# Optimization experiments

Hardware: AMD Instinct MI355X
Metric: run time of the kernel (lower is better)

The kernel has to match this reference:

```python
import jax, jax.numpy as jnp
import numpy as np

EMBED_DIM = 1024
NUM_HEADS = 16
HEAD_DIM = EMBED_DIM // NUM_HEADS
TGT_LEN = 1024
SRC_LEN = 1024
BSZ = 4


def setup_inputs() -> dict:
    key = jax.random.key(0)
    ks = jax.random.split(key, 7)
    query = jax.random.normal(ks[0], (TGT_LEN, BSZ, EMBED_DIM), dtype=jnp.float32)
    key_t = jax.random.normal(ks[1], (SRC_LEN, BSZ, EMBED_DIM), dtype=jnp.float32)
    # hard 0/1 multiplicative mask applied post-softmax
    hard_attention = jax.random.randint(ks[2], (BSZ, TGT_LEN, SRC_LEN), 0, 2).astype(jnp.float32)
    # xavier_uniform_ on [3E, E]
    limit = float(np.sqrt(6.0 / (3 * EMBED_DIM + EMBED_DIM)))
    in_proj_weight = jax.random.uniform(ks[3], (3 * EMBED_DIM, EMBED_DIM), dtype=jnp.float32,
                                        minval=-limit, maxval=limit)
    in_proj_bias = jnp.zeros((3 * EMBED_DIM,), dtype=jnp.float32)
    limit_o = float(np.sqrt(1.0 / EMBED_DIM))
    out_proj_weight = jax.random.uniform(ks[4], (EMBED_DIM, EMBED_DIM), dtype=jnp.float32,
                                         minval=-limit_o, maxval=limit_o)
    out_proj_bias = jnp.zeros((EMBED_DIM,), dtype=jnp.float32)
    return {
        "query": query,
        "key": key_t,
        "hard_attention": hard_attention,
        "in_proj_weight": in_proj_weight,
        "in_proj_bias": in_proj_bias,
        "out_proj_weight": out_proj_weight,
        "out_proj_bias": out_proj_bias,
    }


def reference(query, key, hard_attention, in_proj_weight, in_proj_bias,
              out_proj_weight, out_proj_bias):
    tgt_len, bsz, embed_dim = query.shape
    src_len = key.shape[0]
    h, hd = NUM_HEADS, embed_dim // NUM_HEADS
    scaling = float(hd) ** -0.5

    # QKV projections (F.linear uses y = x @ W.T + b)
    wq = in_proj_weight[:embed_dim]
    wkv = in_proj_weight[embed_dim:]
    bq = in_proj_bias[:embed_dim]
    bkv = in_proj_bias[embed_dim:]
    q = jnp.einsum('tbe,fe->tbf', query, wq) + bq          # [T,B,E]
    kv = jnp.einsum('sbe,fe->sbf', key, wkv) + bkv          # [S,B,2E]
    k, v = jnp.split(kv, 2, axis=-1)

    q = (q * scaling).reshape(tgt_len, bsz, h, hd).transpose(1, 2, 0, 3)  # [B,H,T,D]
    k = k.reshape(src_len, bsz, h, hd).transpose(1, 2, 0, 3)              # [B,H,S,D]
    v = v.reshape(src_len, bsz, h, hd).transpose(1, 2, 0, 3)              # [B,H,S,D]

    scores = jnp.einsum('bhtd,bhsd->bhts', q, k)            # [B,H,T,S]
    attn = jax.nn.softmax(scores, axis=-1)
    # dropout_p = 0.0 -> identity
    attn = attn * hard_attention[:, None, :, :]             # post-softmax hard mask

    out = jnp.einsum('bhts,bhsd->bhtd', attn, v)            # [B,H,T,D]
    out = out.transpose(2, 0, 1, 3).reshape(tgt_len, bsz, embed_dim)
    out = jnp.einsum('tbe,fe->tbf', out, out_proj_weight) + out_proj_bias

    avg_weights = attn.sum(axis=1) / h                      # [B,T,S]
    return (out, avg_weights)
```

## Files before the change

### kernel.cpp

```cpp
#include <hip/hip_runtime.h>
#include <cstdint>
#include <cstddef>

typedef __bf16 bf16x8 __attribute__((ext_vector_type(8)));
typedef float  f32x4  __attribute__((ext_vector_type(4)));
typedef unsigned short u16x8 __attribute__((ext_vector_type(8)));

__device__ __forceinline__ uint16_t f2bf(float f) {
  uint32_t u = __float_as_uint(f);
  u += 0x7fffu + ((u >> 16) & 1u);
  return (uint16_t)(u >> 16);
}
__device__ __forceinline__ float bf2f(uint16_t u) {
  return __uint_as_float((uint32_t)u << 16);
}
__device__ __forceinline__ uint32_t cvtpk(float lo, float hi) {
  uint32_t r;
  asm("v_cvt_pk_bf16_f32 %0, %1, %2" : "=v"(r) : "v"(lo), "v"(hi));
  return r;
}

__device__ __forceinline__ f32x4 mfma16(bf16x8 a, bf16x8 b, f32x4 c) {
  return __builtin_amdgcn_mfma_f32_16x16x32_bf16(a, b, c, 0, 0, 0);
}

#define GLD_TO_LDS16(gptr, lptr)                                                   \
  __builtin_amdgcn_global_load_lds(                                                \
      (const __attribute__((address_space(1))) void*)(gptr),                       \
      (__attribute__((address_space(3))) void*)(lptr), 16, 0, 0)

__global__ void cvt_all(const float* __restrict__ q, const float* __restrict__ k,
                        const float* __restrict__ w, const float* __restrict__ wo,
                        uint16_t* __restrict__ Xq, uint16_t* __restrict__ Xk,
                        uint16_t* __restrict__ Wb, uint16_t* __restrict__ Wob) {
  int i = blockIdx.x * blockDim.x + threadIdx.x;
  const float* src;
  uint16_t* dst;
  int off;
  if (i < 1048576)      { src = q;  dst = Xq;  off = i; }
  else if (i < 2097152) { src = k;  dst = Xk;  off = i - 1048576; }
  else if (i < 2883584) { src = w;  dst = Wb;  off = i - 2097152; }
  else                  { src = wo; dst = Wob; off = i - 2883584; }
  float4 v = ((const float4*)src)[off];
  ushort4 o;
  o.x = f2bf(v.x); o.y = f2bf(v.y); o.z = f2bf(v.z); o.w = f2bf(v.w);
  ((ushort4*)dst)[off] = o;
}

__global__ void bitpack(const float* __restrict__ hard, uint32_t* __restrict__ bits) {
  int i = blockIdx.x * 256 + threadIdx.x;
  unsigned long long m = __ballot(hard[i] != 0.0f);
  if ((threadIdx.x & 63) == 0) {
    int w = i >> 5;
    bits[w]     = (uint32_t)m;
    bits[w + 1] = (uint32_t)(m >> 32);
  }
}

__global__ __launch_bounds__(256)
void gemm_qkv(const uint16_t* __restrict__ Xq, const uint16_t* __restrict__ Xk,
              const uint16_t* __restrict__ Wb, const float* __restrict__ ipb,
              uint16_t* __restrict__ Qb, uint16_t* __restrict__ Kb,
              uint16_t* __restrict__ Vt) {
  __shared__ __align__(16) uint16_t As[128 * 32];
  __shared__ __align__(16) uint16_t Bs[128 * 32];
  const int tid  = threadIdx.x;
  const int wave = tid >> 6, lane = tid & 63;
  const int quad = lane >> 4, l16 = lane & 15;

  const int bid = blockIdx.x;
  const uint16_t *A, *B;
  const float* bias;
  int bm, bn, mode;
  if (bid < 256) {
    mode = 0; A = Xq; B = Wb; bias = ipb;
    bm = bid >> 3; bn = bid & 7;
  } else {
    mode = 1; A = Xk; B = Wb + (1 << 20); bias = ipb + 1024;
    int t = bid - 256; bm = t >> 4; bn = t & 15;
  }
  const int wm = (wave >> 1) << 6, wn = (wave & 1) << 6;
  const int K = 1024;

  f32x4 acc[4][4] = {};

  for (int k0 = 0; k0 < K; k0 += 32) {
    __syncthreads();
#pragma unroll
    for (int j = 0; j < 2; j++) {
      int c   = wave * 128 + j * 64 + lane;
      int row = c >> 2, kc = c & 3;
      const uint16_t* ga = A + (size_t)(bm * 128 + row) * K + k0 + kc * 8;
      GLD_TO_LDS16(ga, As + (size_t)(wave * 128 + j * 64) * 8);
      const uint16_t* gb = B + (size_t)(bn * 128 + row) * K + k0 + kc * 8;
      GLD_TO_LDS16(gb, Bs + (size_t)(wave * 128 + j * 64) * 8);
    }
    __syncthreads();

    bf16x8 af[4], bfr[4];
#pragma unroll
    for (int i = 0; i < 4; i++) {
      af[i]  = *(const bf16x8*)(As + (wm + i * 16 + l16) * 32 + quad * 8);
      bfr[i] = *(const bf16x8*)(Bs + (wn + i * 16 + l16) * 32 + quad * 8);
    }
#pragma unroll
    for (int mi = 0; mi < 4; mi++)
#pragma unroll
      for (int ni = 0; ni < 4; ni++)
        acc[mi][ni] = mfma16(af[mi], bfr[ni], acc[mi][ni]);
  }

#pragma unroll
  for (int mi = 0; mi < 4; mi++)
#pragma unroll
    for (int ni = 0; ni < 4; ni++)
#pragma unroll
      for (int r = 0; r < 4; r++) {
        int gi = bm * 128 + wm + mi * 16 + quad * 4 + r;
        int gf = bn * 128 + wn + ni * 16 + l16;
        float c = acc[mi][ni][r] + bias[gf];
        if (mode == 0) {
          c *= 0.125f;
          int t = gi >> 2, b = gi & 3, h = gf >> 6, d = gf & 63;
          Qb[((((size_t)b * 16 + h) * 1024 + t) << 6) + d] = f2bf(c);
        } else {
          int s = gi >> 2, b = gi & 3;
          if (gf < 1024) {
            int h = gf >> 6, d = gf & 63;
            Kb[((((size_t)b * 16 + h) * 1024 + s) << 6) + d] = f2bf(c);
          } else {
            int fv = gf - 1024, h = fv >> 6, d = fv & 63;
            Vt[((((size_t)b * 16 + h) * 64 + d) << 10) + s] = f2bf(c);
          }
        }
      }
}

__global__ __launch_bounds__(256)
void gemm_out(const uint16_t* __restrict__ A, const uint16_t* __restrict__ B,
              const float* __restrict__ bias, float* __restrict__ o32) {
  __shared__ __align__(16) uint16_t As[64 * 32];
  __shared__ __align__(16) uint16_t Bs[128 * 32];
  const int tid  = threadIdx.x;
  const int wave = tid >> 6, lane = tid & 63;
  const int quad = lane >> 4, l16 = lane & 15;
  const int bm = blockIdx.x >> 3, bn = blockIdx.x & 7;
  const int wm = (wave >> 1) << 5, wn = (wave & 1) << 6;
  const int K = 1024;

  f32x4 acc[2][4] = {};

  for (int k0 = 0; k0 < K; k0 += 32) {
    __syncthreads();
    {
      int c   = wave * 64 + lane;
      int row = c >> 2, kc = c & 3;
      const uint16_t* ga = A + (size_t)(bm * 64 + row) * K + k0 + kc * 8;
      GLD_TO_LDS16(ga, As + (size_t)(wave * 64) * 8);
    }
#pragma unroll
    for (int j = 0; j < 2; j++) {
      int c   = wave * 128 + j * 64 + lane;
      int row = c >> 2, kc = c & 3;
      const uint16_t* gb = B + (size_t)(bn * 128 + row) * K + k0 + kc * 8;
      GLD_TO_LDS16(gb, Bs + (size_t)(wave * 128 + j * 64) * 8);
    }
    __syncthreads();

    bf16x8 af[2], bfr[4];
#pragma unroll
    for (int i = 0; i < 2; i++)
      af[i] = *(const bf16x8*)(As + (wm + i * 16 + l16) * 32 + quad * 8);
#pragma unroll
    for (int i = 0; i < 4; i++)
      bfr[i] = *(const bf16x8*)(Bs + (wn + i * 16 + l16) * 32 + quad * 8);
#pragma unroll
    for (int mi = 0; mi < 2; mi++)
#pragma unroll
      for (int ni = 0; ni < 4; ni++)
        acc[mi][ni] = mfma16(af[mi], bfr[ni], acc[mi][ni]);
  }

#pragma unroll
  for (int mi = 0; mi < 2; mi++)
#pragma unroll
    for (int ni = 0; ni < 4; ni++)
#pragma unroll
      for (int r = 0; r < 4; r++) {
        int gi = bm * 64 + wm + mi * 16 + quad * 4 + r;
        int gf = bn * 128 + wn + ni * 16 + l16;
        o32[(size_t)gi * 1024 + gf] = acc[mi][ni][r] + bias[gf];
      }
}

__global__ __launch_bounds__(256, 2)
void attn_kernel(const uint16_t* __restrict__ qb, const uint16_t* __restrict__ kb,
                 const uint16_t* __restrict__ vtb, const uint32_t* __restrict__ bits,
                 uint16_t* __restrict__ attn_out, float* __restrict__ rlout) {
  __shared__ __align__(16) uint16_t Ks[128 * 64];
  __shared__ __align__(16) uint16_t Vs[64 * 128];
  __shared__ __align__(16) uint16_t Pb[4 * 32 * 128];

  const int bid = blockIdx.x;
  const int xcd = bid & 7, j = bid >> 3;
  const int slab = xcd * 8 + (j >> 3);
  const int b = slab >> 4, h = slab & 15;
  const int t0 = (j & 7) << 7;
  const int tid = threadIdx.x, wave = tid >> 6, lane = tid & 63;
  const int quad = lane >> 4, l16 = lane & 15;
  const int sw = (l16 & 7) << 4;
  const size_t bh = (size_t)b * 16 + h;
  const int tw = t0 + wave * 32;
  const int ta = tw + l16, tb = ta + 16;
  char* PwA = (char*)(Pb + wave * (32 * 128)) + l16 * 256;
  char* PwB = PwA + 16 * 256;

  const uint16_t* qA = qb + ((bh << 10) + ta) * 64;
  bf16x8 aqA0 = *(const bf16x8*)(qA + quad * 8);
  bf16x8 aqA1 = *(const bf16x8*)(qA + 32 + quad * 8);
  bf16x8 aqB0 = *(const bf16x8*)(qA + 1024 + quad * 8);
  bf16x8 aqB1 = *(const bf16x8*)(qA + 1024 + 32 + quad * 8);

  f32x4 accA[4] = {}, accB[4] = {};
  float smA = 0.f, smB = 0.f;

  const int kr = tid >> 3, kc8 = tid & 7;
  const int vr = tid >> 4, vc16 = tid & 15;

  const uint32_t* bA = bits + (((size_t)(b << 10) + ta) << 5);
  const uint32_t* bB = bits + (((size_t)(b << 10) + tb) << 5);

  u16x8 kreg[4], vreg[4];
#pragma unroll
  for (int r = 0; r < 4; r++)
    kreg[r] = *(const u16x8*)(kb + (bh << 16) + (size_t)(r * 256 + tid) * 8);
#pragma unroll
  for (int r = 0; r < 4; r++)
    vreg[r] = *(const u16x8*)(vtb + (((bh << 6) + r * 16 + vr) << 10) + vc16 * 8);
  uint4 uA = *(const uint4*)bA;
  uint4 uB = *(const uint4*)bB;

  for (int sc = 0; sc < 8; sc++) {
    uint32_t wA[4] = {uA.x >> (quad * 4), uA.y >> (quad * 4),
                      uA.z >> (quad * 4), uA.w >> (quad * 4)};
    uint32_t wB[4] = {uB.x >> (quad * 4), uB.y >> (quad * 4),
                      uB.z >> (quad * 4), uB.w >> (quad * 4)};

    __syncthreads();
#pragma unroll
    for (int r = 0; r < 4; r++) {
      const int row = r * 32 + kr;
      *(u16x8*)((char*)Ks + row * 128 + ((kc8 * 16) ^ ((row & 7) << 4))) = kreg[r];
    }
#pragma unroll
    for (int r = 0; r < 4; r++) {
      const int row = r * 16 + vr;
      *(u16x8*)((char*)Vs + row * 256 + ((vc16 * 16) ^ ((row & 7) << 4))) = vreg[r];
    }
    __syncthreads();

    if (sc < 7) {
      const uint16_t* kbase = kb + (bh << 16) + (size_t)(sc + 1) * 8192;
#pragma unroll
      for (int r = 0; r < 4; r++)
        kreg[r] = *(const u16x8*)(kbase + (size_t)(r * 256 + tid) * 8);
#pragma unroll
      for (int r = 0; r < 4; r++)
        vreg[r] = *(const u16x8*)(vtb + (((bh << 6) + r * 16 + vr) << 10) +
                                  (sc + 1) * 128 + vc16 * 8);
      uA = *(const uint4*)(bA + (sc + 1) * 4);
      uB = *(const uint4*)(bB + (sc + 1) * 4);
    }

#pragma unroll
    for (int nn = 0; nn < 8; nn++) {
      const char* kbp = (const char*)Ks + (nn * 16 + l16) * 128;
      bf16x8 bk0 = *(const bf16x8*)(kbp + ((quad * 16) ^ sw));
      bf16x8 bk1 = *(const bf16x8*)(kbp + ((64 + quad * 16) ^ sw));
      f32x4 cA = {}, cB = {};
      cA = mfma16(bk0, aqA0, cA); cA = mfma16(bk1, aqA1, cA);
      cB = mfma16(bk0, aqB0, cB); cB = mfma16(bk1, aqB1, cB);
      const uint32_t mA = wA[nn >> 1] >> ((nn & 1) * 16);
      const uint32_t mB = wB[nn >> 1] >> ((nn & 1) * 16);
      float eA[4], eB[4];
#pragma unroll
      for (int r = 0; r < 4; r++) {
        eA[r] = __expf(cA[r]); smA += eA[r];
        eB[r] = __expf(cB[r]); smB += eB[r];
        eA[r] = ((mA >> r) & 1) ? eA[r] : 0.f;
        eB[r] = ((mB >> r) & 1) ? eB[r] : 0.f;
      }
      const int pc = (nn * 32 + quad * 8) ^ sw;
      *(uint2*)(PwA + pc) = make_uint2(cvtpk(eA[0], eA[1]), cvtpk(eA[2], eA[3]));
      *(uint2*)(PwB + pc) = make_uint2(cvtpk(eB[0], eB[1]), cvtpk(eB[2], eB[3]));
    }

#pragma unroll
    for (int kc = 0; kc < 4; kc++) {
      const int pcb = (kc * 64 + quad * 16) ^ sw;
      bf16x8 apA = *(const bf16x8*)(PwA + pcb);
      bf16x8 apB = *(const bf16x8*)(PwB + pcb);
#pragma unroll
      for (int dt = 0; dt < 4; dt++) {
        bf16x8 bv = *(const bf16x8*)((const char*)Vs + (dt * 16 + l16) * 256 +
                                     ((kc * 64 + quad * 16) ^ sw));
        accA[dt] = mfma16(bv, apA, accA[dt]);
        accB[dt] = mfma16(bv, apB, accB[dt]);
      }
    }
  }

  smA += __shfl_xor(smA, 16); smA += __shfl_xor(smA, 32);
  smB += __shfl_xor(smB, 16); smB += __shfl_xor(smB, 32);
  const float rlA = 1.0f / smA, rlB = 1.0f / smB;
  if (quad == 0) rlout[(bh << 10) + ta] = rlA;
  if (quad == 1) rlout[(bh << 10) + tb] = rlB;

#pragma unroll
  for (int dt = 0; dt < 4; dt++) {
    uint2 oA = make_uint2(cvtpk(accA[dt][0] * rlA, accA[dt][1] * rlA),
                          cvtpk(accA[dt][2] * rlA, accA[dt][3] * rlA));
    *(uint2*)(attn_out + ((size_t)(ta * 4 + b) << 10) + h * 64 + dt * 16 + quad * 4) = oA;
    uint2 oB = make_uint2(cvtpk(accB[dt][0] * rlB, accB[dt][1] * rlB),
                          cvtpk(accB[dt][2] * rlB, accB[dt][3] * rlB));
    *(uint2*)(attn_out + ((size_t)(tb * 4 + b) << 10) + h * 64 + dt * 16 + quad * 4) = oB;
  }
}

__global__ __launch_bounds__(256, 2)
void avg_kernel(const uint16_t* __restrict__ qb, const uint16_t* __restrict__ kb,
                const float* __restrict__ rlin, const uint32_t* __restrict__ bits,
                float* __restrict__ avgout) {
  __shared__ __align__(16) uint16_t Ks[128 * 64];

  const int bid = blockIdx.x;
  const int xcd = bid & 7, j = bid >> 3;
  const int b  = xcd >> 1;
  const int t0 = ((xcd & 1) * 8 + (j >> 3)) << 6;
  const int s0 = (j & 7) << 7;
  const int tid = threadIdx.x, wave = tid >> 6, lane = tid & 63;
  const int quad = lane >> 4, l16 = lane & 15;
  const int sw = (l16 & 7) << 4;
  const int tr = t0 + wave * 16 + l16;
  const int kr = tid >> 3, kc8 = tid & 7;

  uint4 u = *(const uint4*)(bits + (((size_t)(b << 10) + tr) << 5) + (s0 >> 5));
  uint32_t w4[4] = {u.x >> (quad * 4), u.y >> (quad * 4),
                    u.z >> (quad * 4), u.w >> (quad * 4)};

  float av[8][4] = {};

  u16x8 kreg[4];
  {
    const uint16_t* kb0 = kb + ((((size_t)b * 16) << 10) + s0) * 64;
#pragma unroll
    for (int r = 0; r < 4; r++)
      kreg[r] = *(const u16x8*)(kb0 + (size_t)(r * 256 + tid) * 8);
  }

  for (int hh = 0; hh < 16; hh++) {
    __syncthreads();
#pragma unroll
    for (int r = 0; r < 4; r++) {
      const int row = r * 32 + kr;
      *(u16x8*)((char*)Ks + row * 128 + ((kc8 * 16) ^ ((row & 7) << 4))) = kreg[r];
    }
    __syncthreads();
    if (hh < 15) {
      const uint16_t* kb2 = kb + ((((size_t)b * 16 + hh + 1) << 10) + s0) * 64;
#pragma unroll
      for (int r = 0; r < 4; r++)
        kreg[r] = *(const u16x8*)(kb2 + (size_t)(r * 256 + tid) * 8);
    }

    const size_t bh = (size_t)b * 16 + hh;
    const uint16_t* qrow = qb + ((bh << 10) + tr) * 64;
    bf16x8 aq0 = *(const bf16x8*)(qrow + quad * 8);
    bf16x8 aq1 = *(const bf16x8*)(qrow + 32 + quad * 8);
    const float rl = rlin[(bh << 10) + tr];

#pragma unroll
    for (int n = 0; n < 8; n++) {
      const char* kbp = (const char*)Ks + (n * 16 + l16) * 128;
      bf16x8 bk0 = *(const bf16x8*)(kbp + ((quad * 16) ^ sw));
      bf16x8 bk1 = *(const bf16x8*)(kbp + ((64 + quad * 16) ^ sw));
      f32x4 c = {};
      c = mfma16(bk0, aq0, c);
      c = mfma16(bk1, aq1, c);
#pragma unroll
      for (int r = 0; r < 4; r++) av[n][r] += __expf(c[r]) * rl;
    }
  }

  float* orow = avgout + ((size_t)(b << 10) + tr) * 1024 + s0 + quad * 4;
#pragma unroll
  for (int n = 0; n < 8; n++) {
    const uint32_t m = w4[n >> 1] >> ((n & 1) * 16);
    float4 f;
    f.x = av[n][0] * (((m >> 0) & 1) ? 0.0625f : 0.f);
    f.y = av[n][1] * (((m >> 1) & 1) ? 0.0625f : 0.f);
    f.z = av[n][2] * (((m >> 2) & 1) ? 0.0625f : 0.f);
    f.w = av[n][3] * (((m >> 3) & 1) ? 0.0625f : 0.f);
    *(float4*)(orow + n * 16) = f;
  }
}

extern "C" void kernel_launch(void* const* d_in, const int* in_sizes, int n_in,
                              void* d_out, int out_size, void* d_ws, size_t ws_size,
                              hipStream_t stream) {
  const float* query = (const float*)d_in[0];
  const float* key   = (const float*)d_in[1];
  const float* hard  = (const float*)d_in[2];
  const float* ipw   = (const float*)d_in[3];
  const float* ipb   = (const float*)d_in[4];
  const float* opw   = (const float*)d_in[5];
  const float* opb   = (const float*)d_in[6];

  char* ws = (char*)d_ws;
  const size_t MB = 1ull << 20;
  uint16_t* Xq  = (uint16_t*)(ws + 0);
  uint16_t* Xk  = (uint16_t*)(ws + 8 * MB);
  uint16_t* Wb  = (uint16_t*)(ws + 16 * MB);
  uint16_t* Wob = (uint16_t*)(ws + 22 * MB);
  uint16_t* Qb  = (uint16_t*)(ws + 24 * MB);
  uint16_t* Kb  = (uint16_t*)(ws + 32 * MB);
  uint16_t* Vt  = (uint16_t*)(ws + 40 * MB);
  uint16_t* AO  = Xq;

  float* out = (float*)d_out;
  float* avg = out + 4194304;
  uint32_t* bits  = (uint32_t*)out;
  float*    rlbuf = out + 131072;

  cvt_all<<<12288, 256, 0, stream>>>(query, key, ipw, opw, Xq, Xk, Wb, Wob);
  bitpack<<<16384, 256, 0, stream>>>(hard, bits);

  gemm_qkv<<<768, 256, 0, stream>>>(Xq, Xk, Wb, ipb, Qb, Kb, Vt);

  attn_kernel<<<512, 256, 0, stream>>>(Qb, Kb, Vt, bits, AO, rlbuf);

  avg_kernel<<<512, 256, 0, stream>>>(Qb, Kb, rlbuf, bits, avg);

  gemm_out<<<512, 256, 0, stream>>>(AO, Wob, opb, out);
}
```

Baseline: 242.0 us.

## Rewrite QKV GEMM with 256x256 tiles, double-buffered swizzled LDS, and 8 waves

Replaces the 128x128 single-buffered QKV projection GEMM with a 256x256 tile kernel running 8 waves per block. The K dimension is staged in 64-wide tiles through double-buffered LDS with an XOR swizzle, and global-to-LDS prefetch of the next tile is interleaved with MFMA phases. The kernel also raises wave priority during the MFMA phases and remaps block ids for L2 locality. The aim is better operand reuse, fewer global loads, fewer bank conflicts, and load latency hidden behind compute. The cost is that only 192 blocks are launched, which may underfill the GPU, and the 128KB LDS footprint limits occupancy.

```diff
diff --git a/kernel.cpp b/kernel.cpp
--- a/kernel.cpp
+++ b/kernel.cpp
@@ -57,80 +57,131 @@
   }
 }
 
-__global__ __launch_bounds__(256)
-void gemm_qkv(const uint16_t* __restrict__ Xq, const uint16_t* __restrict__ Xk,
-              const uint16_t* __restrict__ Wb, const float* __restrict__ ipb,
-              uint16_t* __restrict__ Qb, uint16_t* __restrict__ Kb,
-              uint16_t* __restrict__ Vt) {
-  __shared__ __align__(16) uint16_t As[128 * 32];
-  __shared__ __align__(16) uint16_t Bs[128 * 32];
+__global__ __launch_bounds__(512, 2)
+void gemm_qkv8(const uint16_t* __restrict__ Xq, const uint16_t* __restrict__ Xk,
+               const uint16_t* __restrict__ Wb, const float* __restrict__ ipb,
+               uint16_t* __restrict__ Qb, uint16_t* __restrict__ Kb,
+               uint16_t* __restrict__ Vt) {
+  __shared__ __align__(16) char lds[131072];
+  char* const Ab0 = lds;
+  char* const Ab1 = lds + 32768;
+  char* const Bb0 = lds + 65536;
+  char* const Bb1 = lds + 98304;
+
   const int tid  = threadIdx.x;
   const int wave = tid >> 6, lane = tid & 63;
   const int quad = lane >> 4, l16 = lane & 15;
-
-  const int bid = blockIdx.x;
-  const uint16_t *A, *B;
+  const int wr = wave >> 2, wc = wave & 3;
+  const int sw = (l16 & 7) << 4;
+
+  const int swz = (blockIdx.x & 7) * 24 + (blockIdx.x >> 3);
+  const uint16_t *Ag, *Bg;
   const float* bias;
   int bm, bn, mode;
-  if (bid < 256) {
-    mode = 0; A = Xq; B = Wb; bias = ipb;
-    bm = bid >> 3; bn = bid & 7;
-  } else {
-    mode = 1; A = Xk; B = Wb + (1 << 20); bias = ipb + 1024;
-    int t = bid - 256; bm = t >> 4; bn = t & 15;
-  }
-  const int wm = (wave >> 1) << 6, wn = (wave & 1) << 6;
-  const int K = 1024;
-
-  f32x4 acc[4][4] = {};
-
-  for (int k0 = 0; k0 < K; k0 += 32) {
-    __syncthreads();
-#pragma unroll
-    for (int j = 0; j < 2; j++) {
-      int c   = wave * 128 + j * 64 + lane;
-      int row = c >> 2, kc = c & 3;
-      const uint16_t* ga = A + (size_t)(bm * 128 + row) * K + k0 + kc * 8;
-      GLD_TO_LDS16(ga, As + (size_t)(wave * 128 + j * 64) * 8);
-      const uint16_t* gb = B + (size_t)(bn * 128 + row) * K + k0 + kc * 8;
-      GLD_TO_LDS16(gb, Bs + (size_t)(wave * 128 + j * 64) * 8);
-    }
-    __syncthreads();
-
-    bf16x8 af[4], bfr[4];
-#pragma unroll
-    for (int i = 0; i < 4; i++) {
-      af[i]  = *(const bf16x8*)(As + (wm + i * 16 + l16) * 32 + quad * 8);
-      bfr[i] = *(const bf16x8*)(Bs + (wn + i * 16 + l16) * 32 + quad * 8);
-    }
-#pragma unroll
-    for (int mi = 0; mi < 4; mi++)
-#pragma unroll
-      for (int ni = 0; ni < 4; ni++)
-        acc[mi][ni] = mfma16(af[mi], bfr[ni], acc[mi][ni]);
-  }
-
-#pragma unroll
-  for (int mi = 0; mi < 4; mi++)
-#pragma unroll
-    for (int ni = 0; ni < 4; ni++)
+  if (swz < 64) { mode = 0; Ag = Xq; Bg = Wb;            bias = ipb;        bm = swz >> 2; bn = swz & 3; }
+  else { int u = swz - 64;
+         mode = 1; Ag = Xk; Bg = Wb + (1 << 20); bias = ipb + 1024; bm = u >> 3;  bn = u & 7; }
+
+  const char* Agb = (const char*)Ag + (size_t)bm * 256 * 2048;
+  const char* Bgb = (const char*)Bg + (size_t)bn * 256 * 2048;
+
+  const int lrow = lane >> 3;
+  const size_t laneoff = (size_t)(wave * 8 + lrow) * 2048 + (((lane & 7) ^ lrow) << 4);
+
+  auto stage = [&](const char* gb, char* lb, int hr, int tk) {
+    GLD_TO_LDS16(gb + (size_t)hr * 131072 + (size_t)tk * 128 + laneoff,
+                 lb + hr * 8192 + wave * 1024);
+  };
+
+  f32x4 acc[8][4] = {};
+  bf16x8 a[4][2], b[2][2][2];
+
+  auto rdA = [&](const char* Ac, int mh) {
+#pragma unroll
+    for (int mi = 0; mi < 4; mi++) {
+      const char* p = Ac + (wr * 128 + mh * 64 + mi * 16 + l16) * 128;
+#pragma unroll
+      for (int ks = 0; ks < 2; ks++)
+        a[mi][ks] = *(const bf16x8*)(p + ((ks * 64 + quad * 16) ^ sw));
+    }
+  };
+  auto rdB = [&](const char* Bc, int nh) {
+#pragma unroll
+    for (int nj = 0; nj < 2; nj++) {
+      const char* p = Bc + (wc * 64 + nh * 32 + nj * 16 + l16) * 128;
+#pragma unroll
+      for (int ks = 0; ks < 2; ks++)
+        b[nh][nj][ks] = *(const bf16x8*)(p + ((ks * 64 + quad * 16) ^ sw));
+    }
+  };
+  auto mm = [&](int mh, int nh) {
+    __builtin_amdgcn_s_setprio(1);
+#pragma unroll
+    for (int ks = 0; ks < 2; ks++)
+#pragma unroll
+      for (int mi = 0; mi < 4; mi++)
+#pragma unroll
+        for (int nj = 0; nj < 2; nj++)
+          acc[mh * 4 + mi][nh * 2 + nj] =
+              mfma16(a[mi][ks], b[nh][nj][ks], acc[mh * 4 + mi][nh * 2 + nj]);
+    __builtin_amdgcn_s_setprio(0);
+  };
+
+  auto ktile = [&](const char* Ac, const char* Bc, char* An, char* Bn,
+                   int tn, bool pf) {
+    rdA(Ac, 0); rdB(Bc, 0);
+    if (pf) { stage(Agb, An, 0, tn); stage(Agb, An, 1, tn); stage(Agb, An, 2, tn); }
+    __builtin_amdgcn_s_barrier();
+    mm(0, 0);
+    __builtin_amdgcn_s_barrier();
+    rdB(Bc, 1);
+    if (pf) { stage(Agb, An, 3, tn); stage(Bgb, Bn, 0, tn); stage(Bgb, Bn, 1, tn); }
+    __builtin_amdgcn_s_barrier();
+    mm(0, 1);
+    __builtin_amdgcn_s_barrier();
+    rdA(Ac, 1);
+    if (pf) { stage(Bgb, Bn, 2, tn); stage(Bgb, Bn, 3, tn); }
+    __builtin_amdgcn_s_barrier();
+    mm(1, 0);
+    __builtin_amdgcn_s_barrier();
+    mm(1, 1);
+    asm volatile("s_waitcnt vmcnt(0)" ::: "memory");
+    __builtin_amdgcn_s_barrier();
+  };
+
+#pragma unroll
+  for (int hr = 0; hr < 4; hr++) stage(Agb, Ab0, hr, 0);
+#pragma unroll
+  for (int hr = 0; hr < 4; hr++) stage(Bgb, Bb0, hr, 0);
+  asm volatile("s_waitcnt vmcnt(0)" ::: "memory");
+  __builtin_amdgcn_s_barrier();
+
+  for (int tt = 0; tt < 16; tt += 2) {
+    ktile(Ab0, Bb0, Ab1, Bb1, tt + 1, true);
+    ktile(Ab1, Bb1, Ab0, Bb0, tt + 2, tt + 2 < 16);
+  }
+
+#pragma unroll
+  for (int mi = 0; mi < 8; mi++)
+#pragma unroll
+    for (int j = 0; j < 4; j++)
 #pragma unroll
       for (int r = 0; r < 4; r++) {
-        int gi = bm * 128 + wm + mi * 16 + quad * 4 + r;
-        int gf = bn * 128 + wn + ni * 16 + l16;
-        float c = acc[mi][ni][r] + bias[gf];
+        int grow = bm * 256 + wr * 128 + mi * 16 + quad * 4 + r;
+        int gf   = bn * 256 + wc * 64 + j * 16 + l16;
+        float c = acc[mi][j][r] + bias[gf];
         if (mode == 0) {
           c *= 0.125f;
-          int t = gi >> 2, b = gi & 3, h = gf >> 6, d = gf & 63;
-          Qb[((((size_t)b * 16 + h) * 1024 + t) << 6) + d] = f2bf(c);
+          int tq = grow >> 2, bb = grow & 3, h = gf >> 6, d = gf & 63;
+          Qb[((((size_t)bb * 16 + h) << 10) + tq) * 64 + d] = f2bf(c);
         } else {
-          int s = gi >> 2, b = gi & 3;
+          int s = grow >> 2, bb = grow & 3;
           if (gf < 1024) {
             int h = gf >> 6, d = gf & 63;
-            Kb[((((size_t)b * 16 + h) * 1024 + s) << 6) + d] = f2bf(c);
+            Kb[((((size_t)bb * 16 + h) << 10) + s) * 64 + d] = f2bf(c);
           } else {
             int fv = gf - 1024, h = fv >> 6, d = fv & 63;
-            Vt[((((size_t)b * 16 + h) * 64 + d) << 10) + s] = f2bf(c);
+            Vt[((((size_t)bb * 16 + h) * 64 + d) << 10) + s] = f2bf(c);
           }
         }
       }
@@ -435,7 +486,7 @@
   cvt_all<<<12288, 256, 0, stream>>>(query, key, ipw, opw, Xq, Xk, Wb, Wob);
   bitpack<<<16384, 256, 0, stream>>>(hard, bits);
 
-  gemm_qkv<<<768, 256, 0, stream>>>(Xq, Xk, Wb, ipb, Qb, Kb, Vt);
+  gemm_qkv8<<<192, 512, 0, stream>>>(Xq, Xk, Wb, ipb, Qb, Kb, Vt);
 
   attn_kernel<<<512, 256, 0, stream>>>(Qb, Kb, Vt, bits, AO, rlbuf);
 
```

After: 251.8 us. 4.0% more time.

## Merge prep kernels and fuse avg-weights with output projection into one tail launch

Applied to the files above, without the earlier changes.

Merges the bf16 conversion and mask bit-packing into one prep launch, and merges the averaged-weights kernel and the output-projection GEMM into one tail kernel whose blocks branch by index. The tail reads the float mask directly instead of the packed bits, because `out` (where the bits live) is now written concurrently. The row-reciprocal buffer moves to workspace for the same reason. It also adds an XCD-aware block swizzle to the QKV GEMM and the out GEMM, and raises tail occupancy via launch bounds. This cuts launch gaps and tail idle time, at the cost of more mask bandwidth in the avg path.

```diff
diff --git a/kernel.cpp b/kernel.cpp
--- a/kernel.cpp
+++ b/kernel.cpp
@@ -29,31 +29,34 @@
       (const __attribute__((address_space(1))) void*)(gptr),                       \
       (__attribute__((address_space(3))) void*)(lptr), 16, 0, 0)
 
-__global__ void cvt_all(const float* __restrict__ q, const float* __restrict__ k,
-                        const float* __restrict__ w, const float* __restrict__ wo,
-                        uint16_t* __restrict__ Xq, uint16_t* __restrict__ Xk,
-                        uint16_t* __restrict__ Wb, uint16_t* __restrict__ Wob) {
-  int i = blockIdx.x * blockDim.x + threadIdx.x;
-  const float* src;
-  uint16_t* dst;
-  int off;
-  if (i < 1048576)      { src = q;  dst = Xq;  off = i; }
-  else if (i < 2097152) { src = k;  dst = Xk;  off = i - 1048576; }
-  else if (i < 2883584) { src = w;  dst = Wb;  off = i - 2097152; }
-  else                  { src = wo; dst = Wob; off = i - 2883584; }
-  float4 v = ((const float4*)src)[off];
-  ushort4 o;
-  o.x = f2bf(v.x); o.y = f2bf(v.y); o.z = f2bf(v.z); o.w = f2bf(v.w);
-  ((ushort4*)dst)[off] = o;
-}
-
-__global__ void bitpack(const float* __restrict__ hard, uint32_t* __restrict__ bits) {
-  int i = blockIdx.x * 256 + threadIdx.x;
-  unsigned long long m = __ballot(hard[i] != 0.0f);
-  if ((threadIdx.x & 63) == 0) {
-    int w = i >> 5;
-    bits[w]     = (uint32_t)m;
-    bits[w + 1] = (uint32_t)(m >> 32);
+__global__ void prep(const float* __restrict__ q, const float* __restrict__ k,
+                     const float* __restrict__ w, const float* __restrict__ wo,
+                     const float* __restrict__ hard,
+                     uint16_t* __restrict__ Xq, uint16_t* __restrict__ Xk,
+                     uint16_t* __restrict__ Wb, uint16_t* __restrict__ Wob,
+                     uint32_t* __restrict__ bits) {
+  const int bid = blockIdx.x;
+  if (bid < 12288) {
+    int i = bid * 256 + threadIdx.x;
+    const float* src;
+    uint16_t* dst;
+    int off;
+    if (i < 1048576)      { src = q;  dst = Xq;  off = i; }
+    else if (i < 2097152) { src = k;  dst = Xk;  off = i - 1048576; }
+    else if (i < 2883584) { src = w;  dst = Wb;  off = i - 2097152; }
+    else                  { src = wo; dst = Wob; off = i - 2883584; }
+    float4 v = ((const float4*)src)[off];
+    ushort4 o;
+    o.x = f2bf(v.x); o.y = f2bf(v.y); o.z = f2bf(v.z); o.w = f2bf(v.w);
+    ((ushort4*)dst)[off] = o;
+  } else {
+    int i = (bid - 12288) * 256 + threadIdx.x;
+    unsigned long long m = __ballot(hard[i] != 0.0f);
+    if ((threadIdx.x & 63) == 0) {
+      int wd = i >> 5;
+      bits[wd]     = (uint32_t)m;
+      bits[wd + 1] = (uint32_t)(m >> 32);
+    }
   }
 }
 
@@ -68,16 +71,16 @@
   const int wave = tid >> 6, lane = tid & 63;
   const int quad = lane >> 4, l16 = lane & 15;
 
-  const int bid = blockIdx.x;
+  const int swz = (blockIdx.x & 7) * 96 + (blockIdx.x >> 3);
   const uint16_t *A, *B;
   const float* bias;
   int bm, bn, mode;
-  if (bid < 256) {
+  if (swz < 256) {
     mode = 0; A = Xq; B = Wb; bias = ipb;
-    bm = bid >> 3; bn = bid & 7;
+    bm = swz >> 3; bn = swz & 7;
   } else {
     mode = 1; A = Xk; B = Wb + (1 << 20); bias = ipb + 1024;
-    int t = bid - 256; bm = t >> 4; bn = t & 15;
+    int t = swz - 256; bm = t >> 4; bn = t & 15;
   }
   const int wm = (wave >> 1) << 6, wn = (wave & 1) << 6;
   const int K = 1024;
@@ -136,63 +139,6 @@
       }
 }
 
-__global__ __launch_bounds__(256)
-void gemm_out(const uint16_t* __restrict__ A, const uint16_t* __restrict__ B,
-              const float* __restrict__ bias, float* __restrict__ o32) {
-  __shared__ __align__(16) uint16_t As[64 * 32];
-  __shared__ __align__(16) uint16_t Bs[128 * 32];
-  const int tid  = threadIdx.x;
-  const int wave = tid >> 6, lane = tid & 63;
-  const int quad = lane >> 4, l16 = lane & 15;
-  const int bm = blockIdx.x >> 3, bn = blockIdx.x & 7;
-  const int wm = (wave >> 1) << 5, wn = (wave & 1) << 6;
-  const int K = 1024;
-
-  f32x4 acc[2][4] = {};
-
-  for (int k0 = 0; k0 < K; k0 += 32) {
-    __syncthreads();
-    {
-      int c   = wave * 64 + lane;
-      int row = c >> 2, kc = c & 3;
-      const uint16_t* ga = A + (size_t)(bm * 64 + row) * K + k0 + kc * 8;
-      GLD_TO_LDS16(ga, As + (size_t)(wave * 64) * 8);
-    }
-#pragma unroll
-    for (int j = 0; j < 2; j++) {
-      int c   = wave * 128 + j * 64 + lane;
-      int row = c >> 2, kc = c & 3;
-      const uint16_t* gb = B + (size_t)(bn * 128 + row) * K + k0 + kc * 8;
-      GLD_TO_LDS16(gb, Bs + (size_t)(wave * 128 + j * 64) * 8);
-    }
-    __syncthreads();
-
-    bf16x8 af[2], bfr[4];
-#pragma unroll
-    for (int i = 0; i < 2; i++)
-      af[i] = *(const bf16x8*)(As + (wm + i * 16 + l16) * 32 + quad * 8);
-#pragma unroll
-    for (int i = 0; i < 4; i++)
-      bfr[i] = *(const bf16x8*)(Bs + (wn + i * 16 + l16) * 32 + quad * 8);
-#pragma unroll
-    for (int mi = 0; mi < 2; mi++)
-#pragma unroll
-      for (int ni = 0; ni < 4; ni++)
-        acc[mi][ni] = mfma16(af[mi], bfr[ni], acc[mi][ni]);
-  }
-
-#pragma unroll
-  for (int mi = 0; mi < 2; mi++)
-#pragma unroll
-    for (int ni = 0; ni < 4; ni++)
-#pragma unroll
-      for (int r = 0; r < 4; r++) {
-        int gi = bm * 64 + wm + mi * 16 + quad * 4 + r;
-        int gf = bn * 128 + wn + ni * 16 + l16;
-        o32[(size_t)gi * 1024 + gf] = acc[mi][ni][r] + bias[gf];
-      }
-}
-
 __global__ __launch_bounds__(256, 2)
 void attn_kernel(const uint16_t* __restrict__ qb, const uint16_t* __restrict__ kb,
                  const uint16_t* __restrict__ vtb, const uint32_t* __restrict__ bits,
@@ -327,81 +273,135 @@
   }
 }
 
-__global__ __launch_bounds__(256, 2)
-void avg_kernel(const uint16_t* __restrict__ qb, const uint16_t* __restrict__ kb,
-                const float* __restrict__ rlin, const uint32_t* __restrict__ bits,
-                float* __restrict__ avgout) {
-  __shared__ __align__(16) uint16_t Ks[128 * 64];
-
+__global__ __launch_bounds__(256, 4)
+void tail(const uint16_t* __restrict__ qb, const uint16_t* __restrict__ kb,
+          const float* __restrict__ rlin, const float* __restrict__ hard,
+          const uint16_t* __restrict__ Ao, const uint16_t* __restrict__ Bw,
+          const float* __restrict__ opb,
+          float* __restrict__ out, float* __restrict__ avgout) {
+  __shared__ __align__(16) char smem[16384];
   const int bid = blockIdx.x;
-  const int xcd = bid & 7, j = bid >> 3;
-  const int b  = xcd >> 1;
-  const int t0 = ((xcd & 1) * 8 + (j >> 3)) << 6;
-  const int s0 = (j & 7) << 7;
   const int tid = threadIdx.x, wave = tid >> 6, lane = tid & 63;
   const int quad = lane >> 4, l16 = lane & 15;
-  const int sw = (l16 & 7) << 4;
-  const int tr = t0 + wave * 16 + l16;
-  const int kr = tid >> 3, kc8 = tid & 7;
-
-  uint4 u = *(const uint4*)(bits + (((size_t)(b << 10) + tr) << 5) + (s0 >> 5));
-  uint32_t w4[4] = {u.x >> (quad * 4), u.y >> (quad * 4),
-                    u.z >> (quad * 4), u.w >> (quad * 4)};
-
-  float av[8][4] = {};
-
-  u16x8 kreg[4];
-  {
-    const uint16_t* kb0 = kb + ((((size_t)b * 16) << 10) + s0) * 64;
-#pragma unroll
-    for (int r = 0; r < 4; r++)
-      kreg[r] = *(const u16x8*)(kb0 + (size_t)(r * 256 + tid) * 8);
-  }
-
-  for (int hh = 0; hh < 16; hh++) {
-    __syncthreads();
-#pragma unroll
-    for (int r = 0; r < 4; r++) {
-      const int row = r * 32 + kr;
-      *(u16x8*)((char*)Ks + row * 128 + ((kc8 * 16) ^ ((row & 7) << 4))) = kreg[r];
-    }
-    __syncthreads();
-    if (hh < 15) {
-      const uint16_t* kb2 = kb + ((((size_t)b * 16 + hh + 1) << 10) + s0) * 64;
+
+  if (bid < 512) {
+    uint16_t* Ks = (uint16_t*)smem;
+    const int xcd = bid & 7, j = bid >> 3;
+    const int b  = xcd >> 1;
+    const int t0 = ((xcd & 1) * 8 + (j >> 3)) << 6;
+    const int s0 = (j & 7) << 7;
+    const int sw = (l16 & 7) << 4;
+    const int tr = t0 + wave * 16 + l16;
+    const int kr = tid >> 3, kc8 = tid & 7;
+
+    float av[8][4] = {};
+
+    u16x8 kreg[4];
+    {
+      const uint16_t* kb0 = kb + ((((size_t)b * 16) << 10) + s0) * 64;
 #pragma unroll
       for (int r = 0; r < 4; r++)
-        kreg[r] = *(const u16x8*)(kb2 + (size_t)(r * 256 + tid) * 8);
-    }
-
-    const size_t bh = (size_t)b * 16 + hh;
-    const uint16_t* qrow = qb + ((bh << 10) + tr) * 64;
-    bf16x8 aq0 = *(const bf16x8*)(qrow + quad * 8);
-    bf16x8 aq1 = *(const bf16x8*)(qrow + 32 + quad * 8);
-    const float rl = rlin[(bh << 10) + tr];
-
+        kreg[r] = *(const u16x8*)(kb0 + (size_t)(r * 256 + tid) * 8);
+    }
+
+    for (int hh = 0; hh < 16; hh++) {
+      __syncthreads();
+#pragma unroll
+      for (int r = 0; r < 4; r++) {
+        const int row = r * 32 + kr;
+        *(u16x8*)((char*)Ks + row * 128 + ((kc8 * 16) ^ ((row & 7) << 4))) = kreg[r];
+      }
+      __syncthreads();
+      if (hh < 15) {
+        const uint16_t* kb2 = kb + ((((size_t)b * 16 + hh + 1) << 10) + s0) * 64;
+#pragma unroll
+        for (int r = 0; r < 4; r++)
+          kreg[r] = *(const u16x8*)(kb2 + (size_t)(r * 256 + tid) * 8);
+      }
+
+      const size_t bh = (size_t)b * 16 + hh;
+      const uint16_t* qrow = qb + ((bh << 10) + tr) * 64;
+      bf16x8 aq0 = *(const bf16x8*)(qrow + quad * 8);
+      bf16x8 aq1 = *(const bf16x8*)(qrow + 32 + quad * 8);
+      const float rl = rlin[(bh << 10) + tr];
+
+#pragma unroll
+      for (int n = 0; n < 8; n++) {
+        const char* kbp = (const char*)Ks + (n * 16 + l16) * 128;
+        bf16x8 bk0 = *(const bf16x8*)(kbp + ((quad * 16) ^ sw));
+        bf16x8 bk1 = *(const bf16x8*)(kbp + ((64 + quad * 16) ^ sw));
+        f32x4 c = {};
+        c = mfma16(bk0, aq0, c);
+        c = mfma16(bk1, aq1, c);
+#pragma unroll
+        for (int r = 0; r < 4; r++) av[n][r] += __expf(c[r]) * rl;
+      }
+    }
+
+    const float* hrow = hard + (((size_t)(b << 10) + tr) << 10) + s0 + quad * 4;
+    float* orow = avgout + ((size_t)(b << 10) + tr) * 1024 + s0 + quad * 4;
 #pragma unroll
     for (int n = 0; n < 8; n++) {
-      const char* kbp = (const char*)Ks + (n * 16 + l16) * 128;
-      bf16x8 bk0 = *(const bf16x8*)(kbp + ((quad * 16) ^ sw));
-      bf16x8 bk1 = *(const bf16x8*)(kbp + ((64 + quad * 16) ^ sw));
-      f32x4 c = {};
-      c = mfma16(bk0, aq0, c);
-      c = mfma16(bk1, aq1, c);
-#pragma unroll
-      for (int r = 0; r < 4; r++) av[n][r] += __expf(c[r]) * rl;
-    }
-  }
-
-  float* orow = avgout + ((size_t)(b << 10) + tr) * 1024 + s0 + quad * 4;
-#pragma unroll
-  for (int n = 0; n < 8; n++) {
-    const uint32_t m = w4[n >> 1] >> ((n & 1) * 16);
-    float4 f;
-    f.x = av[n][0] * (((m >> 0) & 1) ? 0.0625f : 0.f);
-    f.y = av[n][1] * (((m >> 1) & 1) ? 0.0625f : 0.f);
-    f.z = av[n][2] * (((m >> 2) & 1) ? 0.0625f : 0.f);
-    f.w = av[n][3] * (((m >> 3) & 1) ? 0.0625f : 0.f);
-    *(float4*)(orow + n * 16) = f;
+      float4 hm = *(const float4*)(hrow + n * 16);
+      float4 f;
+      f.x = av[n][0] * (hm.x != 0.f ? 0.0625f : 0.f);
+      f.y = av[n][1] * (hm.y != 0.f ? 0.0625f : 0.f);
+      f.z = av[n][2] * (hm.z != 0.f ? 0.0625f : 0.f);
+      f.w = av[n][3] * (hm.w != 0.f ? 0.0625f : 0.f);
+      *(float4*)(orow + n * 16) = f;
+    }
+  } else {
+    uint16_t* As = (uint16_t*)smem;
+    uint16_t* Bs = (uint16_t*)(smem + 4096);
+    const int u = bid - 512;
+    const int swz = (u & 7) * 64 + (u >> 3);
+    const int bm = swz >> 3, bn = swz & 7;
+    const int wm = (wave >> 1) << 5, wn = (wave & 1) << 6;
+    const int K = 1024;
+
+    f32x4 acc[2][4] = {};
+
+    for (int k0 = 0; k0 < K; k0 += 32) {
+      __syncthreads();
+      {
+        int c   = wave * 64 + lane;
+        int row = c >> 2, kc = c & 3;
+        const uint16_t* ga = Ao + (size_t)(bm * 64 + row) * K + k0 + kc * 8;
+        GLD_TO_LDS16(ga, As + (size_t)(wave * 64) * 8);
+      }
+#pragma unroll
+      for (int jj = 0; jj < 2; jj++) {
+        int c   = wave * 128 + jj * 64 + lane;
+        int row = c >> 2, kc = c & 3;
+        const uint16_t* gb = Bw + (size_t)(bn * 128 + row) * K + k0 + kc * 8;
+        GLD_TO_LDS16(gb, Bs + (size_t)(wave * 128 + jj * 64) * 8);
+      }
+      __syncthreads();
+
+      bf16x8 af[2], bfr[4];
+#pragma unroll
+      for (int i = 0; i < 2; i++)
+        af[i] = *(const bf16x8*)(As + (wm + i * 16 + l16) * 32 + quad * 8);
+#pragma unroll
+      for (int i = 0; i < 4; i++)
+        bfr[i] = *(const bf16x8*)(Bs + (wn + i * 16 + l16) * 32 + quad * 8);
+#pragma unroll
+      for (int mi = 0; mi < 2; mi++)
+#pragma unroll
+        for (int ni = 0; ni < 4; ni++)
+          acc[mi][ni] = mfma16(af[mi], bfr[ni], acc[mi][ni]);
+    }
+
+#pragma unroll
+    for (int mi = 0; mi < 2; mi++)
+#pragma unroll
+      for (int ni = 0; ni < 4; ni++)
+#pragma unroll
+        for (int r = 0; r < 4; r++) {
+          int gi = bm * 64 + wm + mi * 16 + quad * 4 + r;
+          int gf = bn * 128 + wn + ni * 16 + l16;
+          out[(size_t)gi * 1024 + gf] = acc[mi][ni][r] + opb[gf];
+        }
   }
 }
 
@@ -426,20 +426,18 @@
   uint16_t* Kb  = (uint16_t*)(ws + 32 * MB);
   uint16_t* Vt  = (uint16_t*)(ws + 40 * MB);
   uint16_t* AO  = Xq;
+  float*    rlws = (float*)(ws + 8 * MB);
 
   float* out = (float*)d_out;
   float* avg = out + 4194304;
-  uint32_t* bits  = (uint32_t*)out;
-  float*    rlbuf = out + 131072;
-
-  cvt_all<<<12288, 256, 0, stream>>>(query, key, ipw, opw, Xq, Xk, Wb, Wob);
-  bitpack<<<16384, 256, 0, stream>>>(hard, bits);
+  uint32_t* bits = (uint32_t*)out;
+
+  prep<<<28672, 256, 0, stream>>>(query, key, ipw, opw, hard,
+                                  Xq, Xk, Wb, Wob, bits);
 
   gemm_qkv<<<768, 256, 0, stream>>>(Xq, Xk, Wb, ipb, Qb, Kb, Vt);
 
-  attn_kernel<<<512, 256, 0, stream>>>(Qb, Kb, Vt, bits, AO, rlbuf);
-
-  avg_kernel<<<512, 256, 0, stream>>>(Qb, Kb, rlbuf, bits, avg);
-
-  gemm_out<<<512, 256, 0, stream>>>(AO, Wob, opb, out);
-}
+  attn_kernel<<<512, 256, 0, stream>>>(Qb, Kb, Vt, bits, AO, rlws);
+
+  tail<<<1024, 256, 0, stream>>>(Qb, Kb, rlws, hard, AO, Wob, opb, out, avg);
+}
```

Result: faster. 229.7 us (-5.1%).
